# Performance work log

Hardware: AMD Instinct MI355X
Metric: run time of the kernel (lower is better)

The kernel has to match this reference:

```python
import jax, jax.numpy as jnp
import numpy as np

DIM = 2048
N_HEADS = 16
N_KV_HEADS = 4
HEAD_DIM = DIM // N_HEADS  # 128
T = 2048


def setup_inputs() -> dict:
    key = jax.random.key(0)
    k1, k2, k3 = jax.random.split(key, 3)
    scale = 1.0 / np.sqrt(DIM)
    x = jax.random.normal(k1, (T, DIM), dtype=jnp.float32)
    # GQA-consistent fused QKV projection: q (n_h*hd) + k (n_kv*hd) + v (n_kv*hd)
    qkv_out = (N_HEADS + 2 * N_KV_HEADS) * HEAD_DIM  # 3072
    W_qkv = jax.random.normal(k2, (DIM, qkv_out), dtype=jnp.float32) * scale
    W_o = jax.random.normal(k3, (N_HEADS * HEAD_DIM, DIM), dtype=jnp.float32) * scale
    return {"x": x, "W_qkv": W_qkv, "W_o": W_o}


def reference(x, W_qkv, W_o):
    Tn, C = x.shape
    hd = HEAD_DIM
    qkv = x @ W_qkv  # [T, (n_h + 2*n_kv)*hd]
    q, k, v = jnp.split(qkv, [N_HEADS * hd, (N_HEADS + N_KV_HEADS) * hd], axis=-1)
    q = q.reshape(Tn, N_HEADS, hd).transpose(1, 0, 2)      # [n_h, T, hd]
    k = k.reshape(Tn, N_KV_HEADS, hd).transpose(1, 0, 2)   # [n_kv, T, hd]
    v = v.reshape(Tn, N_KV_HEADS, hd).transpose(1, 0, 2)
    rep = N_HEADS // N_KV_HEADS
    k = jnp.repeat(k, rep, axis=0)  # [n_h, T, hd]
    v = jnp.repeat(v, rep, axis=0)
    scores = jnp.einsum('hid,hjd->hij', q, k) / jnp.sqrt(jnp.asarray(hd, x.dtype))
    causal = jnp.tril(jnp.ones((Tn, Tn), dtype=bool))[None, :, :]
    scores = jnp.where(causal, scores, -jnp.inf)
    attn = jax.nn.softmax(scores, axis=-1)
    out = jnp.einsum('hij,hjd->hid', attn, v)  # [n_h, T, hd]
    out = out.transpose(1, 0, 2).reshape(Tn, N_HEADS * hd)
    return out @ W_o
```

## Files before the change

### kernel.cpp

```cpp
#include <hip/hip_runtime.h>
#include <stdint.h>

#define T_SEQ   2048
#define DMODEL  2048
#define NH      16
#define HD      128
#define QKVN    3072
#define KCOL    2048
#define VCOL    2560

typedef __bf16 bf16x8 __attribute__((ext_vector_type(8)));
typedef float  f32x4  __attribute__((ext_vector_type(4)));
typedef unsigned short u16x8 __attribute__((ext_vector_type(8)));

__device__ __forceinline__ uint16_t f2bf(float f) {
    uint32_t u = __builtin_bit_cast(uint32_t, f);
    u += 0x7fffu + ((u >> 16) & 1u);
    return (uint16_t)(u >> 16);
}
__device__ __forceinline__ float bf2f(uint16_t u) {
    return __builtin_bit_cast(float, (uint32_t)u << 16);
}
__device__ __forceinline__ u16x8 ld8(const uint16_t* p) {
    return *reinterpret_cast<const u16x8*>(p);
}
__device__ __forceinline__ void st8(uint16_t* p, u16x8 v) {
    *reinterpret_cast<u16x8*>(p) = v;
}
__device__ __forceinline__ bf16x8 as_bf(u16x8 v) { return __builtin_bit_cast(bf16x8, v); }

__device__ __forceinline__ uint32_t cvtpk(float a, float b) {
    uint32_t r;
    asm("v_cvt_pk_bf16_f32 %0, %1, %2" : "=v"(r) : "v"(a), "v"(b));
    return r;
}

__device__ __forceinline__ void gl_lds16(const uint16_t* g, uint16_t* l) {
    __builtin_amdgcn_global_load_lds((const __attribute__((address_space(1))) void*)g,
                                     (__attribute__((address_space(3))) void*)l, 16, 0, 0);
}

__global__ __launch_bounds__(256) void k_cast(const float* __restrict__ in,
                                              uint16_t* __restrict__ out, int n8) {
    int i = blockIdx.x * 256 + threadIdx.x;
    if (i >= n8) return;
    const f32x4* p = reinterpret_cast<const f32x4*>(in) + (size_t)i * 2;
    f32x4 a = p[0], b = p[1];
    u16x8 o;
    o[0] = f2bf(a[0]); o[1] = f2bf(a[1]); o[2] = f2bf(a[2]); o[3] = f2bf(a[3]);
    o[4] = f2bf(b[0]); o[5] = f2bf(b[1]); o[6] = f2bf(b[2]); o[7] = f2bf(b[3]);
    reinterpret_cast<u16x8*>(out)[i] = o;
}

__global__ __launch_bounds__(256) void k_tcast(const float* __restrict__ in,
                                               uint16_t* __restrict__ out, int R, int C) {
    __shared__ uint16_t tile[64][72];
    int t = threadIdx.x;
    int rbase = blockIdx.y * 64, cbase = blockIdx.x * 64;
#pragma unroll
    for (int p = 0; p < 4; ++p) {
        int ir = p * 16 + (t >> 4);
        int ic = (t & 15) * 4;
        f32x4 v = *reinterpret_cast<const f32x4*>(&in[(size_t)(rbase + ir) * C + cbase + ic]);
        tile[ir][ic + 0] = f2bf(v[0]);
        tile[ir][ic + 1] = f2bf(v[1]);
        tile[ir][ic + 2] = f2bf(v[2]);
        tile[ir][ic + 3] = f2bf(v[3]);
    }
    __syncthreads();
#pragma unroll
    for (int p = 0; p < 2; ++p) {
        int oc = p * 32 + (t >> 3);
        int orr = (t & 7) * 8;
        u16x8 o;
#pragma unroll
        for (int e = 0; e < 8; ++e) o[e] = tile[orr + e][oc];
        st8(&out[(size_t)(cbase + oc) * R + rbase + orr], o);
    }
}

__global__ __launch_bounds__(256) void k_tbf16(const uint16_t* __restrict__ in,
                                               uint16_t* __restrict__ out,
                                               int R, int C, int ldin, int coff) {
    __shared__ uint16_t tile[64][72];
    int t = threadIdx.x;
    int rbase = blockIdx.y * 64, cbase = blockIdx.x * 64;
#pragma unroll
    for (int p = 0; p < 2; ++p) {
        int ir = p * 32 + (t >> 3);
        int ic = (t & 7) * 8;
        u16x8 v = ld8(&in[(size_t)(rbase + ir) * ldin + coff + cbase + ic]);
#pragma unroll
        for (int e = 0; e < 8; ++e) tile[ir][ic + e] = v[e];
    }
    __syncthreads();
#pragma unroll
    for (int p = 0; p < 2; ++p) {
        int oc = p * 32 + (t >> 3);
        int orr = (t & 7) * 8;
        u16x8 o;
#pragma unroll
        for (int e = 0; e < 8; ++e) o[e] = tile[orr + e][oc];
        st8(&out[(size_t)(cbase + oc) * R + rbase + orr], o);
    }
}

__global__ __launch_bounds__(256) void k_gemm(const uint16_t* __restrict__ A,
                                              const uint16_t* __restrict__ Bt,
                                              void* __restrict__ Cout,
                                              int M, int N, int K, int gy,
                                              int out_bf16, int scale_cols, float qscale) {
    __shared__ __align__(16) uint16_t Asm[2][64 * 64];
    __shared__ __align__(16) uint16_t Bsm[2][128 * 64];
    int t = threadIdx.x;
    int w = t >> 6, lane = t & 63, lo = lane & 15, g4 = lane >> 4;

    int nwg = (int)gridDim.x;
    int wg = (int)blockIdx.x;
    int idx = (wg & 7) * (nwg >> 3) + (wg >> 3);
    int bx = idx / gy, by = idx % gy;
    int mbase = by * 64, nbase = bx * 128;

    int wm = w >> 1, wn = w & 1;

    const uint16_t* pA[2]; int lofsA[2];
#pragma unroll
    for (int c = 0; c < 2; ++c) {
        int ch = w * 2 + c;
        int r = ch * 8 + (lane >> 3);
        pA[c] = A + (size_t)(mbase + r) * K + (((lane & 7) ^ (r & 7)) * 8);
        lofsA[c] = ch * 512;
    }
    const uint16_t* pB[4]; int lofsB[4];
#pragma unroll
    for (int c = 0; c < 4; ++c) {
        int ch = w * 4 + c;
        int r = ch * 8 + (lane >> 3);
        pB[c] = Bt + (size_t)(nbase + r) * K + (((lane & 7) ^ (r & 7)) * 8);
        lofsB[c] = ch * 512;
    }

    f32x4 acc[2][4] = {};

#pragma unroll
    for (int c = 0; c < 2; ++c) gl_lds16(pA[c], &Asm[0][lofsA[c]]);
#pragma unroll
    for (int c = 0; c < 4; ++c) gl_lds16(pB[c], &Bsm[0][lofsB[c]]);

    int cur = 0;
    for (int kt = 0; kt < K; kt += 64) {
        __syncthreads();
        if (kt + 64 < K) {
            int ko = kt + 64;
#pragma unroll
            for (int c = 0; c < 2; ++c) gl_lds16(pA[c] + ko, &Asm[cur ^ 1][lofsA[c]]);
#pragma unroll
            for (int c = 0; c < 4; ++c) gl_lds16(pB[c] + ko, &Bsm[cur ^ 1][lofsB[c]]);
        }
        bf16x8 af[2][2], bfr[2][4];
#pragma unroll
        for (int ks = 0; ks < 2; ++ks) {
#pragma unroll
            for (int i = 0; i < 2; ++i) {
                int ar = wm * 32 + i * 16 + lo;
                af[ks][i] = as_bf(ld8(&Asm[cur][(ar * 64 + ks * 32 + g4 * 8) ^ ((lo & 7) << 3)]));
            }
#pragma unroll
            for (int j = 0; j < 4; ++j) {
                int br = wn * 64 + j * 16 + lo;
                bfr[ks][j] = as_bf(ld8(&Bsm[cur][(br * 64 + ks * 32 + g4 * 8) ^ ((lo & 7) << 3)]));
            }
        }
        __builtin_amdgcn_s_setprio(1);
#pragma unroll
        for (int ks = 0; ks < 2; ++ks)
#pragma unroll
            for (int i = 0; i < 2; ++i)
#pragma unroll
                for (int j = 0; j < 4; ++j)
                    acc[i][j] = __builtin_amdgcn_mfma_f32_16x16x32_bf16(af[ks][i], bfr[ks][j], acc[i][j], 0, 0, 0);
        __builtin_amdgcn_s_setprio(0);
        cur ^= 1;
    }

    if (out_bf16) {
        uint16_t* C = (uint16_t*)Cout;
#pragma unroll
        for (int i = 0; i < 2; ++i)
#pragma unroll
            for (int j = 0; j < 4; ++j)
#pragma unroll
                for (int r = 0; r < 4; ++r) {
                    int row = mbase + wm * 32 + i * 16 + g4 * 4 + r;
                    int col = nbase + wn * 64 + j * 16 + lo;
                    float v = acc[i][j][r];
                    if (col < scale_cols) v *= qscale;
                    C[(size_t)row * N + col] = f2bf(v);
                }
    } else {
        float* C = (float*)Cout;
#pragma unroll
        for (int i = 0; i < 2; ++i)
#pragma unroll
            for (int j = 0; j < 4; ++j)
#pragma unroll
                for (int r = 0; r < 4; ++r) {
                    int row = mbase + wm * 32 + i * 16 + g4 * 4 + r;
                    int col = nbase + wn * 64 + j * 16 + lo;
                    C[(size_t)row * N + col] = acc[i][j][r];
                }
    }
}

__global__ __launch_bounds__(256) void k_attn(const uint16_t* __restrict__ qkv,
                                              const uint16_t* __restrict__ vt,
                                              uint16_t* __restrict__ po,
                                              float* __restrict__ pml) {
    __shared__ __align__(16) uint16_t Ksm[2][64 * 128];
    __shared__ __align__(16) uint16_t Vsm[2][128 * 64];
    __shared__ __align__(16) uint16_t Psm[4][16 * 72];
    int t = threadIdx.x;
    int w = t >> 6, lane = t & 63, lo = lane & 15, g4 = lane >> 4;
    int x = blockIdx.x, h = blockIdx.y, p = blockIdx.z, kh = h >> 2;

    const uint16_t* kbase = qkv + KCOL + (size_t)kh * HD;
    const uint16_t* vbase = vt + (size_t)(kh * HD) * T_SEQ;

    const uint16_t* kp[4]; const uint16_t* vp[4]; int lofs[4];
#pragma unroll
    for (int c = 0; c < 4; ++c) {
        int ch = w * 4 + c;
        int kr = ch * 4 + (lane >> 4);
        kp[c] = kbase + (size_t)kr * QKVN + ((lane & 15) ^ (kr & 7)) * 8;
        int vr = ch * 8 + (lane >> 3);
        vp[c] = vbase + (size_t)vr * T_SEQ + ((lane & 7) ^ (vr & 7)) * 8;
        lofs[c] = ch * 512;
    }

    for (int rep = 0; rep < 2; ++rep) {
        int qt = rep ? 31 - x : x;
        int qb = qt * 64;
        int cnt = (qt + 2 - p) >> 1;

        bf16x8 qf[4];
        {
            int qrow = qb + w * 16 + lo;
            const uint16_t* qp = &qkv[(size_t)qrow * QKVN + h * HD + g4 * 8];
#pragma unroll
            for (int ks = 0; ks < 4; ++ks) qf[ks] = as_bf(ld8(qp + ks * 32));
        }

        f32x4 o[8] = {};
        float mr = -INFINITY, pp = 0.f;

        if (cnt) {
            __syncthreads();
            size_t ko = (size_t)p * 64 * QKVN; int vo = p * 64;
#pragma unroll
            for (int c = 0; c < 4; ++c) {
                gl_lds16(kp[c] + ko, &Ksm[0][lofs[c]]);
                gl_lds16(vp[c] + vo, &Vsm[0][lofs[c]]);
            }
        }

        int cur = 0;
        for (int it = 0; it < cnt; ++it) {
            int jt = p + 2 * it;
            __syncthreads();
            if (it + 1 < cnt) {
                size_t ko = (size_t)(jt + 2) * 64 * QKVN;
                int vo = (jt + 2) * 64;
#pragma unroll
                for (int c = 0; c < 4; ++c) {
                    gl_lds16(kp[c] + ko, &Ksm[cur ^ 1][lofs[c]]);
                    gl_lds16(vp[c] + vo, &Vsm[cur ^ 1][lofs[c]]);
                }
            }

            f32x4 s[4] = {};
            __builtin_amdgcn_s_setprio(1);
#pragma unroll
            for (int nt = 0; nt < 4; ++nt) {
                int j = nt * 16 + lo;
#pragma unroll
                for (int ks = 0; ks < 4; ++ks) {
                    bf16x8 a = as_bf(ld8(&Ksm[cur][(j * 128 + ks * 32 + g4 * 8) ^ ((lo & 7) << 3)]));
                    s[nt] = __builtin_amdgcn_mfma_f32_16x16x32_bf16(a, qf[ks], s[nt], 0, 0, 0);
                }
            }
            __builtin_amdgcn_s_setprio(0);

            if (jt == qt) {
                int i = qb + w * 16 + lo;
                int jb = jt * 64;
#pragma unroll
                for (int nt = 0; nt < 4; ++nt)
#pragma unroll
                    for (int r = 0; r < 4; ++r) {
                        int j = jb + nt * 16 + g4 * 4 + r;
                        if (j > i) s[nt][r] = -INFINITY;
                    }
            }

            float pm = fmaxf(
                fmaxf(fmaxf(fmaxf(s[0][0], s[0][1]), fmaxf(s[0][2], s[0][3])),
                      fmaxf(fmaxf(s[1][0], s[1][1]), fmaxf(s[1][2], s[1][3]))),
                fmaxf(fmaxf(fmaxf(s[2][0], s[2][1]), fmaxf(s[2][2], s[2][3])),
                      fmaxf(fmaxf(s[3][0], s[3][1]), fmaxf(s[3][2], s[3][3]))));
            pm = fmaxf(pm, __shfl_xor(pm, 16));
            pm = fmaxf(pm, __shfl_xor(pm, 32));

            if (__any(pm > mr + 11.f)) {
                float mn = fmaxf(mr, pm);
                float al = exp2f(fminf(fmaxf(mr, -1e30f) - mn, 0.f));
                mr = mn;
                pp *= al;
                float alo[4];
#pragma unroll
                for (int r = 0; r < 4; ++r)
                    alo[r] = __shfl(al, (lane & 48) | (((lane >> 4) << 2) + r));
#pragma unroll
                for (int dt = 0; dt < 8; ++dt)
#pragma unroll
                    for (int r = 0; r < 4; ++r) o[dt][r] *= alo[r];
            }
            float msafe = fmaxf(mr, -1e30f);
#pragma unroll
            for (int nt = 0; nt < 4; ++nt)
#pragma unroll
                for (int r = 0; r < 4; ++r) {
                    float pe = exp2f(s[nt][r] - msafe);
                    s[nt][r] = pe;
                    pp += pe;
                }
#pragma unroll
            for (int nt = 0; nt < 4; ++nt) {
                uint32_t p01 = cvtpk(s[nt][0], s[nt][1]);
                uint32_t p23 = cvtpk(s[nt][2], s[nt][3]);
                *reinterpret_cast<uint2*>(&Psm[w][lo * 72 + nt * 16 + g4 * 4]) =
                    make_uint2(p01, p23);
            }

            __builtin_amdgcn_s_setprio(1);
#pragma unroll
            for (int ks2 = 0; ks2 < 2; ++ks2) {
                bf16x8 pa = as_bf(ld8(&Psm[w][lo * 72 + ks2 * 32 + g4 * 8]));
#pragma unroll
                for (int dt = 0; dt < 8; ++dt) {
                    int d = dt * 16 + lo;
                    bf16x8 vb = as_bf(ld8(&Vsm[cur][(d * 64 + ks2 * 32 + g4 * 8) ^ ((lo & 7) << 3)]));
                    o[dt] = __builtin_amdgcn_mfma_f32_16x16x32_bf16(pa, vb, o[dt], 0, 0, 0);
                }
            }
            __builtin_amdgcn_s_setprio(0);
            cur ^= 1;
        }

        float lr = pp;
        lr += __shfl_xor(lr, 16);
        lr += __shfl_xor(lr, 32);

        uint16_t* pob = po + (size_t)p * T_SEQ * DMODEL;
#pragma unroll
        for (int dt = 0; dt < 8; ++dt)
#pragma unroll
            for (int r = 0; r < 4; ++r) {
                int i = qb + w * 16 + g4 * 4 + r;
                int col = h * HD + dt * 16 + lo;
                pob[(size_t)i * DMODEL + col] = f2bf(o[dt][r]);
            }
        if (lane < 16) {
            int i = qb + w * 16 + lane;
            float* pe = pml + (size_t)p * T_SEQ * NH * 2 + ((size_t)i * NH + h) * 2;
            pe[0] = mr;
            pe[1] = lr;
        }
    }
}

__global__ __launch_bounds__(256) void k_comb(uint16_t* __restrict__ po,
                                              const float* __restrict__ pml) {
    int i = blockIdx.x * 256 + threadIdx.x;
    int row = i >> 8;
    int cg = i & 255;
    int h = cg >> 4;
    int col = cg * 8;
    const size_t PS = (size_t)T_SEQ * NH * 2;
    const size_t TD = (size_t)T_SEQ * DMODEL;
    size_t mo = ((size_t)row * NH + h) * 2;
    float m0 = pml[mo], l0 = pml[mo + 1];
    float m1 = pml[PS + mo], l1 = pml[PS + mo + 1];
    float m = fmaxf(m0, m1);
    float w0 = exp2f(m0 - m), w1 = exp2f(m1 - m);
    float rl = 1.f / (l0 * w0 + l1 * w1);
    size_t off = (size_t)row * DMODEL + col;
    u16x8 a = ld8(po + off);
    u16x8 b = ld8(po + TD + off);
    u16x8 o;
#pragma unroll
    for (int e = 0; e < 8; ++e)
        o[e] = f2bf((bf2f(a[e]) * w0 + bf2f(b[e]) * w1) * rl);
    st8(po + off, o);
}

extern "C" void kernel_launch(void* const* d_in, const int* in_sizes, int n_in,
                              void* d_out, int out_size, void* d_ws, size_t ws_size,
                              hipStream_t stream) {
    (void)in_sizes; (void)n_in; (void)out_size; (void)ws_size;
    const float* x    = (const float*)d_in[0];
    const float* Wqkv = (const float*)d_in[1];
    const float* Wo   = (const float*)d_in[2];
    float* out = (float*)d_out;

    char* ws = (char*)d_ws;
    uint16_t* xb   = (uint16_t*)(ws + 0);
    uint16_t* wqt  = (uint16_t*)(ws + 8388608);
    uint16_t* po   = (uint16_t*)(ws + 0);
    float*    pml  = (float*)(ws + 16777216);
    uint16_t* wot  = (uint16_t*)(ws + 20971520);
    uint16_t* qkvb = (uint16_t*)(ws + 29360128);
    uint16_t* vtb  = (uint16_t*)(ws + 41943040);

    const float qscale = 0.12751743f;

    k_cast<<<2048, 256, 0, stream>>>(x, xb, 524288);
    k_tcast<<<dim3(48, 32), 256, 0, stream>>>(Wqkv, wqt, 2048, 3072);
    k_tcast<<<dim3(32, 32), 256, 0, stream>>>(Wo, wot, 2048, 2048);
    k_gemm<<<768, 256, 0, stream>>>(xb, wqt, qkvb, 2048, 3072, 2048, 32, 1, 2048, qscale);
    k_tbf16<<<dim3(8, 32), 256, 0, stream>>>(qkvb, vtb, 2048, 512, 3072, 2560);
    k_attn<<<dim3(16, 16, 2), 256, 0, stream>>>(qkvb, vtb, po, pml);
    k_comb<<<2048, 256, 0, stream>>>(po, pml);
    k_gemm<<<512, 256, 0, stream>>>(po, wot, out, 2048, 2048, 2048, 32, 0, 0, 1.0f);
}
```

Before: 133.7 us.

## Triple-buffer GEMM LDS with K-tile 32 and vmcnt-based barrier

Changes the GEMM's shared-memory pipeline from double buffering with 64-wide K tiles to triple buffering with 32-wide K tiles. Loads now run two stages ahead, and the full __syncthreads is replaced by a partial s_waitcnt vmcnt(3) plus a raw barrier. The swizzle is redone for the narrower 32-element rows. The goal is to hide global-load latency better while using less LDS per block. The cost is twice as many loop iterations and barriers per K, with fewer MFMAs between each sync.

```diff
diff --git a/kernel.cpp b/kernel.cpp
--- a/kernel.cpp
+++ b/kernel.cpp
@@ -110,8 +110,8 @@
                                               void* __restrict__ Cout,
                                               int M, int N, int K, int gy,
                                               int out_bf16, int scale_cols, float qscale) {
-    __shared__ __align__(16) uint16_t Asm[2][64 * 64];
-    __shared__ __align__(16) uint16_t Bsm[2][128 * 64];
+    __shared__ __align__(16) uint16_t Asm[3][64 * 32];
+    __shared__ __align__(16) uint16_t Bsm[3][128 * 32];
     int t = threadIdx.x;
     int w = t >> 6, lane = t & 63, lo = lane & 15, g4 = lane >> 4;
 
@@ -123,64 +123,79 @@
 
     int wm = w >> 1, wn = w & 1;
 
-    const uint16_t* pA[2]; int lofsA[2];
+    int rA = w * 16 + (lane >> 2);
+    const uint16_t* pA = A + (size_t)(mbase + rA) * K + (((lane & 3) ^ ((rA >> 1) & 3)) * 8);
+    int lofsA = w * 512;
+    const uint16_t* pB[2]; int lofsB[2];
 #pragma unroll
     for (int c = 0; c < 2; ++c) {
         int ch = w * 2 + c;
-        int r = ch * 8 + (lane >> 3);
-        pA[c] = A + (size_t)(mbase + r) * K + (((lane & 7) ^ (r & 7)) * 8);
-        lofsA[c] = ch * 512;
-    }
-    const uint16_t* pB[4]; int lofsB[4];
-#pragma unroll
-    for (int c = 0; c < 4; ++c) {
-        int ch = w * 4 + c;
-        int r = ch * 8 + (lane >> 3);
-        pB[c] = Bt + (size_t)(nbase + r) * K + (((lane & 7) ^ (r & 7)) * 8);
+        int r = ch * 16 + (lane >> 2);
+        pB[c] = Bt + (size_t)(nbase + r) * K + (((lane & 3) ^ ((r >> 1) & 3)) * 8);
         lofsB[c] = ch * 512;
     }
 
     f32x4 acc[2][4] = {};
-
-#pragma unroll
-    for (int c = 0; c < 2; ++c) gl_lds16(pA[c], &Asm[0][lofsA[c]]);
-#pragma unroll
-    for (int c = 0; c < 4; ++c) gl_lds16(pB[c], &Bsm[0][lofsB[c]]);
-
-    int cur = 0;
-    for (int kt = 0; kt < K; kt += 64) {
-        __syncthreads();
-        if (kt + 64 < K) {
-            int ko = kt + 64;
-#pragma unroll
-            for (int c = 0; c < 2; ++c) gl_lds16(pA[c] + ko, &Asm[cur ^ 1][lofsA[c]]);
-#pragma unroll
-            for (int c = 0; c < 4; ++c) gl_lds16(pB[c] + ko, &Bsm[cur ^ 1][lofsB[c]]);
-        }
-        bf16x8 af[2][2], bfr[2][4];
-#pragma unroll
-        for (int ks = 0; ks < 2; ++ks) {
-#pragma unroll
-            for (int i = 0; i < 2; ++i) {
-                int ar = wm * 32 + i * 16 + lo;
-                af[ks][i] = as_bf(ld8(&Asm[cur][(ar * 64 + ks * 32 + g4 * 8) ^ ((lo & 7) << 3)]));
-            }
-#pragma unroll
-            for (int j = 0; j < 4; ++j) {
-                int br = wn * 64 + j * 16 + lo;
-                bfr[ks][j] = as_bf(ld8(&Bsm[cur][(br * 64 + ks * 32 + g4 * 8) ^ ((lo & 7) << 3)]));
-            }
+    int nt = K >> 5;
+
+    gl_lds16(pA, &Asm[0][lofsA]);
+    gl_lds16(pB[0], &Bsm[0][lofsB[0]]); gl_lds16(pB[1], &Bsm[0][lofsB[1]]);
+    gl_lds16(pA + 32, &Asm[1][lofsA]);
+    gl_lds16(pB[0] + 32, &Bsm[1][lofsB[0]]); gl_lds16(pB[1] + 32, &Bsm[1][lofsB[1]]);
+
+    int cur = 0, st = 2;
+    for (int tt = 0; tt < nt - 1; ++tt) {
+        asm volatile("s_waitcnt vmcnt(3)" ::: "memory");
+        __builtin_amdgcn_s_barrier();
+        asm volatile("" ::: "memory");
+        if (tt + 2 < nt) {
+            int ko = (tt + 2) * 32;
+            gl_lds16(pA + ko, &Asm[st][lofsA]);
+            gl_lds16(pB[0] + ko, &Bsm[st][lofsB[0]]);
+            gl_lds16(pB[1] + ko, &Bsm[st][lofsB[1]]);
+        }
+        bf16x8 af[2], bfr[4];
+#pragma unroll
+        for (int i = 0; i < 2; ++i) {
+            int ar = wm * 32 + i * 16 + lo;
+            af[i] = as_bf(ld8(&Asm[cur][(ar * 32 + g4 * 8) ^ (((ar >> 1) & 3) << 3)]));
+        }
+#pragma unroll
+        for (int j = 0; j < 4; ++j) {
+            int br = wn * 64 + j * 16 + lo;
+            bfr[j] = as_bf(ld8(&Bsm[cur][(br * 32 + g4 * 8) ^ (((br >> 1) & 3) << 3)]));
         }
         __builtin_amdgcn_s_setprio(1);
 #pragma unroll
-        for (int ks = 0; ks < 2; ++ks)
-#pragma unroll
-            for (int i = 0; i < 2; ++i)
-#pragma unroll
-                for (int j = 0; j < 4; ++j)
-                    acc[i][j] = __builtin_amdgcn_mfma_f32_16x16x32_bf16(af[ks][i], bfr[ks][j], acc[i][j], 0, 0, 0);
+        for (int i = 0; i < 2; ++i)
+#pragma unroll
+            for (int j = 0; j < 4; ++j)
+                acc[i][j] = __builtin_amdgcn_mfma_f32_16x16x32_bf16(af[i], bfr[j], acc[i][j], 0, 0, 0);
         __builtin_amdgcn_s_setprio(0);
-        cur ^= 1;
+        asm volatile("" ::: "memory");
+        cur = (cur == 2) ? 0 : cur + 1;
+        st  = (st  == 2) ? 0 : st  + 1;
+    }
+    asm volatile("s_waitcnt vmcnt(0)" ::: "memory");
+    __builtin_amdgcn_s_barrier();
+    asm volatile("" ::: "memory");
+    {
+        bf16x8 af[2], bfr[4];
+#pragma unroll
+        for (int i = 0; i < 2; ++i) {
+            int ar = wm * 32 + i * 16 + lo;
+            af[i] = as_bf(ld8(&Asm[cur][(ar * 32 + g4 * 8) ^ (((ar >> 1) & 3) << 3)]));
+        }
+#pragma unroll
+        for (int j = 0; j < 4; ++j) {
+            int br = wn * 64 + j * 16 + lo;
+            bfr[j] = as_bf(ld8(&Bsm[cur][(br * 32 + g4 * 8) ^ (((br >> 1) & 3) << 3)]));
+        }
+#pragma unroll
+        for (int i = 0; i < 2; ++i)
+#pragma unroll
+            for (int j = 0; j < 4; ++j)
+                acc[i][j] = __builtin_amdgcn_mfma_f32_16x16x32_bf16(af[i], bfr[j], acc[i][j], 0, 0, 0);
     }
 
     if (out_bf16) {
```

Result: slower. 146.1 us (+9.3%).

## Enlarge attention query tile to 128 rows per block with single-buffered K

Applied to the files above, without the earlier changes.

Each attention block now covers 128 query rows, with each wave owning two 16-row halves, instead of looping over two balanced 64-row tiles. Every K/V tile loaded into shared memory now serves twice as many queries, which cuts shared-memory and global traffic per unit of work. K drops to a single buffer that is refilled after an extra mid-iteration barrier, and the PV MFMA operands are swapped so output stores are vectorized. In exchange, register pressure roughly doubles for the accumulators, blocks no longer get balanced causal work (heaviest blocks are scheduled first), and the added barrier may expose K load latency.

```diff
diff --git a/kernel.cpp b/kernel.cpp
--- a/kernel.cpp
+++ b/kernel.cpp
@@ -216,12 +216,15 @@
                                               const uint16_t* __restrict__ vt,
                                               uint16_t* __restrict__ po,
                                               float* __restrict__ pml) {
-    __shared__ __align__(16) uint16_t Ksm[2][64 * 128];
+    __shared__ __align__(16) uint16_t Ksm[64 * 128];
     __shared__ __align__(16) uint16_t Vsm[2][128 * 64];
-    __shared__ __align__(16) uint16_t Psm[4][16 * 72];
+    __shared__ __align__(16) uint16_t Psm[4][32 * 72];
     int t = threadIdx.x;
     int w = t >> 6, lane = t & 63, lo = lane & 15, g4 = lane >> 4;
-    int x = blockIdx.x, h = blockIdx.y, p = blockIdx.z, kh = h >> 2;
+    int qt1 = 15 - (int)blockIdx.x;
+    int h = blockIdx.y, p = blockIdx.z, kh = h >> 2;
+    int qb = qt1 * 128;
+    int qwb = w * 32;
 
     const uint16_t* kbase = qkv + KCOL + (size_t)kh * HD;
     const uint16_t* vbase = vt + (size_t)(kh * HD) * T_SEQ;
@@ -237,143 +240,165 @@
         lofs[c] = ch * 512;
     }
 
-    for (int rep = 0; rep < 2; ++rep) {
-        int qt = rep ? 31 - x : x;
-        int qb = qt * 64;
-        int cnt = (qt + 2 - p) >> 1;
-
-        bf16x8 qf[4];
-        {
-            int qrow = qb + w * 16 + lo;
-            const uint16_t* qp = &qkv[(size_t)qrow * QKVN + h * HD + g4 * 8];
-#pragma unroll
-            for (int ks = 0; ks < 4; ++ks) qf[ks] = as_bf(ld8(qp + ks * 32));
-        }
-
-        f32x4 o[8] = {};
-        float mr = -INFINITY, pp = 0.f;
-
-        if (cnt) {
-            __syncthreads();
-            size_t ko = (size_t)p * 64 * QKVN; int vo = p * 64;
-#pragma unroll
-            for (int c = 0; c < 4; ++c) {
-                gl_lds16(kp[c] + ko, &Ksm[0][lofs[c]]);
-                gl_lds16(vp[c] + vo, &Vsm[0][lofs[c]]);
-            }
-        }
-
-        int cur = 0;
-        for (int it = 0; it < cnt; ++it) {
-            int jt = p + 2 * it;
-            __syncthreads();
-            if (it + 1 < cnt) {
-                size_t ko = (size_t)(jt + 2) * 64 * QKVN;
-                int vo = (jt + 2) * 64;
-#pragma unroll
-                for (int c = 0; c < 4; ++c) {
-                    gl_lds16(kp[c] + ko, &Ksm[cur ^ 1][lofs[c]]);
-                    gl_lds16(vp[c] + vo, &Vsm[cur ^ 1][lofs[c]]);
-                }
-            }
-
-            f32x4 s[4] = {};
-            __builtin_amdgcn_s_setprio(1);
-#pragma unroll
-            for (int nt = 0; nt < 4; ++nt) {
-                int j = nt * 16 + lo;
-#pragma unroll
-                for (int ks = 0; ks < 4; ++ks) {
-                    bf16x8 a = as_bf(ld8(&Ksm[cur][(j * 128 + ks * 32 + g4 * 8) ^ ((lo & 7) << 3)]));
-                    s[nt] = __builtin_amdgcn_mfma_f32_16x16x32_bf16(a, qf[ks], s[nt], 0, 0, 0);
-                }
-            }
-            __builtin_amdgcn_s_setprio(0);
-
-            if (jt == qt) {
-                int i = qb + w * 16 + lo;
-                int jb = jt * 64;
-#pragma unroll
-                for (int nt = 0; nt < 4; ++nt)
+    bf16x8 qf[2][4];
+#pragma unroll
+    for (int qh = 0; qh < 2; ++qh) {
+        const uint16_t* qp = &qkv[(size_t)(qb + qwb + qh * 16 + lo) * QKVN + h * HD + g4 * 8];
+#pragma unroll
+        for (int ks = 0; ks < 4; ++ks) qf[qh][ks] = as_bf(ld8(qp + ks * 32));
+    }
+
+    f32x4 o[2][8] = {};
+    float mr[2] = {-INFINITY, -INFINITY}, pp[2] = {0.f, 0.f};
+    int cnt = qt1 + 1;
+
+    {
+        size_t ko = (size_t)p * 64 * QKVN; int vo = p * 64;
+#pragma unroll
+        for (int c = 0; c < 4; ++c) {
+            gl_lds16(kp[c] + ko, &Ksm[lofs[c]]);
+            gl_lds16(vp[c] + vo, &Vsm[0][lofs[c]]);
+        }
+    }
+
+    int cur = 0;
+    for (int it = 0; it < cnt; ++it) {
+        int jt = p + 2 * it;
+        __syncthreads();
+        if (it + 1 < cnt) {
+            int vo = (jt + 2) * 64;
+#pragma unroll
+            for (int c = 0; c < 4; ++c) gl_lds16(vp[c] + vo, &Vsm[cur ^ 1][lofs[c]]);
+        }
+
+        f32x4 s[4][2] = {};
+        __builtin_amdgcn_s_setprio(1);
+#pragma unroll
+        for (int nt = 0; nt < 4; ++nt) {
+            int j = nt * 16 + lo;
+#pragma unroll
+            for (int ks = 0; ks < 4; ++ks) {
+                bf16x8 a = as_bf(ld8(&Ksm[(j * 128 + ks * 32 + g4 * 8) ^ ((lo & 7) << 3)]));
+                s[nt][0] = __builtin_amdgcn_mfma_f32_16x16x32_bf16(a, qf[0][ks], s[nt][0], 0, 0, 0);
+                s[nt][1] = __builtin_amdgcn_mfma_f32_16x16x32_bf16(a, qf[1][ks], s[nt][1], 0, 0, 0);
+            }
+        }
+        __builtin_amdgcn_s_setprio(0);
+
+        asm volatile("" ::: "memory");
+        __builtin_amdgcn_s_barrier();
+        asm volatile("" ::: "memory");
+        if (it + 1 < cnt) {
+            size_t ko = (size_t)(jt + 2) * 64 * QKVN;
+#pragma unroll
+            for (int c = 0; c < 4; ++c) gl_lds16(kp[c] + ko, &Ksm[lofs[c]]);
+        }
+
+        if (jt >= 2 * qt1) {
+            int jb = jt * 64;
+#pragma unroll
+            for (int nt = 0; nt < 4; ++nt)
+#pragma unroll
+                for (int qh = 0; qh < 2; ++qh) {
+                    int i = qb + qwb + qh * 16 + lo;
 #pragma unroll
                     for (int r = 0; r < 4; ++r) {
                         int j = jb + nt * 16 + g4 * 4 + r;
-                        if (j > i) s[nt][r] = -INFINITY;
+                        if (j > i) s[nt][qh][r] = -INFINITY;
                     }
-            }
-
-            float pm = fmaxf(
-                fmaxf(fmaxf(fmaxf(s[0][0], s[0][1]), fmaxf(s[0][2], s[0][3])),
-                      fmaxf(fmaxf(s[1][0], s[1][1]), fmaxf(s[1][2], s[1][3]))),
-                fmaxf(fmaxf(fmaxf(s[2][0], s[2][1]), fmaxf(s[2][2], s[2][3])),
-                      fmaxf(fmaxf(s[3][0], s[3][1]), fmaxf(s[3][2], s[3][3]))));
-            pm = fmaxf(pm, __shfl_xor(pm, 16));
-            pm = fmaxf(pm, __shfl_xor(pm, 32));
-
-            if (__any(pm > mr + 11.f)) {
-                float mn = fmaxf(mr, pm);
-                float al = exp2f(fminf(fmaxf(mr, -1e30f) - mn, 0.f));
-                mr = mn;
-                pp *= al;
-                float alo[4];
-#pragma unroll
-                for (int r = 0; r < 4; ++r)
-                    alo[r] = __shfl(al, (lane & 48) | (((lane >> 4) << 2) + r));
-#pragma unroll
-                for (int dt = 0; dt < 8; ++dt)
-#pragma unroll
-                    for (int r = 0; r < 4; ++r) o[dt][r] *= alo[r];
-            }
-            float msafe = fmaxf(mr, -1e30f);
+                }
+        }
+
+        float pm[2];
+#pragma unroll
+        for (int qh = 0; qh < 2; ++qh) {
+            float m01 = fmaxf(fmaxf(fmaxf(s[0][qh][0], s[0][qh][1]), fmaxf(s[0][qh][2], s[0][qh][3])),
+                              fmaxf(fmaxf(s[1][qh][0], s[1][qh][1]), fmaxf(s[1][qh][2], s[1][qh][3])));
+            float m23 = fmaxf(fmaxf(fmaxf(s[2][qh][0], s[2][qh][1]), fmaxf(s[2][qh][2], s[2][qh][3])),
+                              fmaxf(fmaxf(s[3][qh][0], s[3][qh][1]), fmaxf(s[3][qh][2], s[3][qh][3])));
+            float pmv = fmaxf(m01, m23);
+            pmv = fmaxf(pmv, __shfl_xor(pmv, 16));
+            pmv = fmaxf(pmv, __shfl_xor(pmv, 32));
+            pm[qh] = pmv;
+        }
+        bool grow = (pm[0] > mr[0] + 11.f) || (pm[1] > mr[1] + 11.f);
+        if (__any(grow)) {
+#pragma unroll
+            for (int qh = 0; qh < 2; ++qh) {
+                float mn = fmaxf(mr[qh], pm[qh]);
+                float al = exp2f(fminf(fmaxf(mr[qh], -1e30f) - mn, 0.f));
+                mr[qh] = mn;
+                pp[qh] *= al;
+#pragma unroll
+                for (int dt = 0; dt < 8; ++dt) o[qh][dt] *= al;
+            }
+        }
+#pragma unroll
+        for (int qh = 0; qh < 2; ++qh) {
+            float msafe = fmaxf(mr[qh], -1e30f);
 #pragma unroll
             for (int nt = 0; nt < 4; ++nt)
 #pragma unroll
                 for (int r = 0; r < 4; ++r) {
-                    float pe = exp2f(s[nt][r] - msafe);
-                    s[nt][r] = pe;
-                    pp += pe;
+                    float pe = exp2f(s[nt][qh][r] - msafe);
+                    s[nt][qh][r] = pe;
+                    pp[qh] += pe;
                 }
+        }
+#pragma unroll
+        for (int qh = 0; qh < 2; ++qh)
 #pragma unroll
             for (int nt = 0; nt < 4; ++nt) {
-                uint32_t p01 = cvtpk(s[nt][0], s[nt][1]);
-                uint32_t p23 = cvtpk(s[nt][2], s[nt][3]);
-                *reinterpret_cast<uint2*>(&Psm[w][lo * 72 + nt * 16 + g4 * 4]) =
+                uint32_t p01 = cvtpk(s[nt][qh][0], s[nt][qh][1]);
+                uint32_t p23 = cvtpk(s[nt][qh][2], s[nt][qh][3]);
+                *reinterpret_cast<uint2*>(&Psm[w][(qh * 16 + lo) * 72 + nt * 16 + g4 * 4]) =
                     make_uint2(p01, p23);
             }
 
-            __builtin_amdgcn_s_setprio(1);
-#pragma unroll
-            for (int ks2 = 0; ks2 < 2; ++ks2) {
-                bf16x8 pa = as_bf(ld8(&Psm[w][lo * 72 + ks2 * 32 + g4 * 8]));
-#pragma unroll
-                for (int dt = 0; dt < 8; ++dt) {
-                    int d = dt * 16 + lo;
-                    bf16x8 vb = as_bf(ld8(&Vsm[cur][(d * 64 + ks2 * 32 + g4 * 8) ^ ((lo & 7) << 3)]));
-                    o[dt] = __builtin_amdgcn_mfma_f32_16x16x32_bf16(pa, vb, o[dt], 0, 0, 0);
-                }
-            }
-            __builtin_amdgcn_s_setprio(0);
-            cur ^= 1;
-        }
-
-        float lr = pp;
-        lr += __shfl_xor(lr, 16);
-        lr += __shfl_xor(lr, 32);
-
-        uint16_t* pob = po + (size_t)p * T_SEQ * DMODEL;
-#pragma unroll
-        for (int dt = 0; dt < 8; ++dt)
-#pragma unroll
-            for (int r = 0; r < 4; ++r) {
-                int i = qb + w * 16 + g4 * 4 + r;
-                int col = h * HD + dt * 16 + lo;
-                pob[(size_t)i * DMODEL + col] = f2bf(o[dt][r]);
-            }
-        if (lane < 16) {
-            int i = qb + w * 16 + lane;
+        __builtin_amdgcn_s_setprio(1);
+#pragma unroll
+        for (int ks2 = 0; ks2 < 2; ++ks2) {
+            bf16x8 pa0 = as_bf(ld8(&Psm[w][(lo) * 72 + ks2 * 32 + g4 * 8]));
+            bf16x8 pa1 = as_bf(ld8(&Psm[w][(16 + lo) * 72 + ks2 * 32 + g4 * 8]));
+#pragma unroll
+            for (int dt = 0; dt < 8; ++dt) {
+                int d = dt * 16 + lo;
+                bf16x8 vb = as_bf(ld8(&Vsm[cur][(d * 64 + ks2 * 32 + g4 * 8) ^ ((lo & 7) << 3)]));
+                o[0][dt] = __builtin_amdgcn_mfma_f32_16x16x32_bf16(vb, pa0, o[0][dt], 0, 0, 0);
+                o[1][dt] = __builtin_amdgcn_mfma_f32_16x16x32_bf16(vb, pa1, o[1][dt], 0, 0, 0);
+            }
+        }
+        __builtin_amdgcn_s_setprio(0);
+        cur ^= 1;
+    }
+
+    float lr[2];
+#pragma unroll
+    for (int qh = 0; qh < 2; ++qh) {
+        float ps = pp[qh];
+        ps += __shfl_xor(ps, 16);
+        ps += __shfl_xor(ps, 32);
+        lr[qh] = ps;
+    }
+
+    uint16_t* pob = po + (size_t)p * T_SEQ * DMODEL;
+#pragma unroll
+    for (int qh = 0; qh < 2; ++qh) {
+        size_t rowo = (size_t)(qb + qwb + qh * 16 + lo) * DMODEL + h * HD + g4 * 4;
+#pragma unroll
+        for (int dt = 0; dt < 8; ++dt) {
+            uint32_t c01 = cvtpk(o[qh][dt][0], o[qh][dt][1]);
+            uint32_t c23 = cvtpk(o[qh][dt][2], o[qh][dt][3]);
+            *reinterpret_cast<uint2*>(&pob[rowo + dt * 16]) = make_uint2(c01, c23);
+        }
+    }
+    if (lane < 16) {
+#pragma unroll
+        for (int qh = 0; qh < 2; ++qh) {
+            int i = qb + qwb + qh * 16 + lane;
             float* pe = pml + (size_t)p * T_SEQ * NH * 2 + ((size_t)i * NH + h) * 2;
-            pe[0] = mr;
-            pe[1] = lr;
+            pe[0] = mr[qh];
+            pe[1] = lr[qh];
         }
     }
 }
```

Measured after the change: 171.7 us. 28.5% more time.

## Rework attention to 128-row Q tiles with 32x32 MFMA and 4-way KV split

Applied to the files above, without the earlier changes.

The attention kernel now processes 128 query rows per block, 32 per wave, using 32x32x16 bf16 MFMA instead of 16x16x32. The key dimension is split four ways instead of two, and the split order is reversed on the second pass to balance causal work. K now uses a single LDS buffer reloaded after a mid-iteration barrier, while V stays double-buffered. The combine kernel merges four partials, and the workspace layout is reshuffled, with the Wo transpose moved later so its buffer can overlap freed space. Larger tiles improve reuse of K/V loads, at the cost of more partial-output traffic, an extra barrier per iteration and more registers per thread.

```diff
diff --git a/kernel.cpp b/kernel.cpp
--- a/kernel.cpp
+++ b/kernel.cpp
@@ -11,6 +11,7 @@
 
 typedef __bf16 bf16x8 __attribute__((ext_vector_type(8)));
 typedef float  f32x4  __attribute__((ext_vector_type(4)));
+typedef float  f32x16 __attribute__((ext_vector_type(16)));
 typedef unsigned short u16x8 __attribute__((ext_vector_type(8)));
 
 __device__ __forceinline__ uint16_t f2bf(float f) {
@@ -216,11 +217,12 @@
                                               const uint16_t* __restrict__ vt,
                                               uint16_t* __restrict__ po,
                                               float* __restrict__ pml) {
-    __shared__ __align__(16) uint16_t Ksm[2][64 * 128];
+    __shared__ __align__(16) uint16_t Ksm[64 * 128];
     __shared__ __align__(16) uint16_t Vsm[2][128 * 64];
-    __shared__ __align__(16) uint16_t Psm[4][16 * 72];
+    __shared__ __align__(16) uint16_t Psm[4][32 * 72];
     int t = threadIdx.x;
-    int w = t >> 6, lane = t & 63, lo = lane & 15, g4 = lane >> 4;
+    int w = t >> 6, lane = t & 63;
+    int q32 = lane & 31, hi = lane >> 5;
     int x = blockIdx.x, h = blockIdx.y, p = blockIdx.z, kh = h >> 2;
 
     const uint16_t* kbase = qkv + KCOL + (size_t)kh * HD;
@@ -238,76 +240,80 @@
     }
 
     for (int rep = 0; rep < 2; ++rep) {
-        int qt = rep ? 31 - x : x;
-        int qb = qt * 64;
-        int cnt = (qt + 2 - p) >> 1;
-
-        bf16x8 qf[4];
+        int qt = rep ? 15 - x : x;
+        int pr = rep ? 3 - p : p;
+        int qb = qt * 128;
+        int cnt = (2 * qt + 5 - pr) >> 2;
+
+        bf16x8 qf[8];
         {
-            int qrow = qb + w * 16 + lo;
-            const uint16_t* qp = &qkv[(size_t)qrow * QKVN + h * HD + g4 * 8];
-#pragma unroll
-            for (int ks = 0; ks < 4; ++ks) qf[ks] = as_bf(ld8(qp + ks * 32));
-        }
-
-        f32x4 o[8] = {};
+            const uint16_t* qp = &qkv[(size_t)(qb + w * 32 + q32) * QKVN + h * HD + hi * 8];
+#pragma unroll
+            for (int ks = 0; ks < 8; ++ks) qf[ks] = as_bf(ld8(qp + ks * 16));
+        }
+
+        f32x16 o[4] = {};
         float mr = -INFINITY, pp = 0.f;
 
         if (cnt) {
             __syncthreads();
-            size_t ko = (size_t)p * 64 * QKVN; int vo = p * 64;
+            size_t ko = (size_t)pr * 64 * QKVN; int vo = pr * 64;
 #pragma unroll
             for (int c = 0; c < 4; ++c) {
-                gl_lds16(kp[c] + ko, &Ksm[0][lofs[c]]);
+                gl_lds16(kp[c] + ko, &Ksm[lofs[c]]);
                 gl_lds16(vp[c] + vo, &Vsm[0][lofs[c]]);
             }
         }
 
         int cur = 0;
         for (int it = 0; it < cnt; ++it) {
-            int jt = p + 2 * it;
+            int jt = pr + 4 * it;
             __syncthreads();
             if (it + 1 < cnt) {
-                size_t ko = (size_t)(jt + 2) * 64 * QKVN;
-                int vo = (jt + 2) * 64;
-#pragma unroll
-                for (int c = 0; c < 4; ++c) {
-                    gl_lds16(kp[c] + ko, &Ksm[cur ^ 1][lofs[c]]);
-                    gl_lds16(vp[c] + vo, &Vsm[cur ^ 1][lofs[c]]);
+                int vo = (jt + 4) * 64;
+#pragma unroll
+                for (int c = 0; c < 4; ++c) gl_lds16(vp[c] + vo, &Vsm[cur ^ 1][lofs[c]]);
+            }
+
+            f32x16 s0 = {}, s1 = {};
+            __builtin_amdgcn_s_setprio(1);
+#pragma unroll
+            for (int ks = 0; ks < 8; ++ks) {
+                int j0 = q32;
+                bf16x8 k0 = as_bf(ld8(&Ksm[(j0 * 128 + ks * 16 + hi * 8) ^ ((j0 & 7) << 3)]));
+                s0 = __builtin_amdgcn_mfma_f32_32x32x16_bf16(k0, qf[ks], s0, 0, 0, 0);
+                int j1 = 32 + q32;
+                bf16x8 k1 = as_bf(ld8(&Ksm[(j1 * 128 + ks * 16 + hi * 8) ^ ((j1 & 7) << 3)]));
+                s1 = __builtin_amdgcn_mfma_f32_32x32x16_bf16(k1, qf[ks], s1, 0, 0, 0);
+            }
+            __builtin_amdgcn_s_setprio(0);
+
+            asm volatile("" ::: "memory");
+            __builtin_amdgcn_s_barrier();
+            asm volatile("" ::: "memory");
+            if (it + 1 < cnt) {
+                size_t ko = (size_t)(jt + 4) * 64 * QKVN;
+#pragma unroll
+                for (int c = 0; c < 4; ++c) gl_lds16(kp[c] + ko, &Ksm[lofs[c]]);
+            }
+
+            if (jt >= 2 * qt) {
+                int i = qb + w * 32 + q32;
+                int jb = jt * 64;
+#pragma unroll
+                for (int r = 0; r < 16; ++r) {
+                    int jr = jb + (r & 3) + 8 * (r >> 2) + 4 * hi;
+                    if (jr > i) s0[r] = -INFINITY;
+                    if (jr + 32 > i) s1[r] = -INFINITY;
                 }
             }
 
-            f32x4 s[4] = {};
-            __builtin_amdgcn_s_setprio(1);
-#pragma unroll
-            for (int nt = 0; nt < 4; ++nt) {
-                int j = nt * 16 + lo;
-#pragma unroll
-                for (int ks = 0; ks < 4; ++ks) {
-                    bf16x8 a = as_bf(ld8(&Ksm[cur][(j * 128 + ks * 32 + g4 * 8) ^ ((lo & 7) << 3)]));
-                    s[nt] = __builtin_amdgcn_mfma_f32_16x16x32_bf16(a, qf[ks], s[nt], 0, 0, 0);
-                }
-            }
-            __builtin_amdgcn_s_setprio(0);
-
-            if (jt == qt) {
-                int i = qb + w * 16 + lo;
-                int jb = jt * 64;
-#pragma unroll
-                for (int nt = 0; nt < 4; ++nt)
-#pragma unroll
-                    for (int r = 0; r < 4; ++r) {
-                        int j = jb + nt * 16 + g4 * 4 + r;
-                        if (j > i) s[nt][r] = -INFINITY;
-                    }
-            }
-
-            float pm = fmaxf(
-                fmaxf(fmaxf(fmaxf(s[0][0], s[0][1]), fmaxf(s[0][2], s[0][3])),
-                      fmaxf(fmaxf(s[1][0], s[1][1]), fmaxf(s[1][2], s[1][3]))),
-                fmaxf(fmaxf(fmaxf(s[2][0], s[2][1]), fmaxf(s[2][2], s[2][3])),
-                      fmaxf(fmaxf(s[3][0], s[3][1]), fmaxf(s[3][2], s[3][3]))));
-            pm = fmaxf(pm, __shfl_xor(pm, 16));
+            float t8[8];
+#pragma unroll
+            for (int r = 0; r < 8; ++r)
+                t8[r] = fmaxf(fmaxf(s0[r], s0[r + 8]), fmaxf(s1[r], s1[r + 8]));
+            float pm = fmaxf(fmaxf(fmaxf(t8[0], t8[1]), fmaxf(t8[2], t8[3])),
+                             fmaxf(fmaxf(t8[4], t8[5]), fmaxf(t8[6], t8[7])));
             pm = fmaxf(pm, __shfl_xor(pm, 32));
 
             if (__any(pm > mr + 11.f)) {
@@ -315,63 +321,68 @@
                 float al = exp2f(fminf(fmaxf(mr, -1e30f) - mn, 0.f));
                 mr = mn;
                 pp *= al;
-                float alo[4];
-#pragma unroll
-                for (int r = 0; r < 4; ++r)
-                    alo[r] = __shfl(al, (lane & 48) | (((lane >> 4) << 2) + r));
-#pragma unroll
-                for (int dt = 0; dt < 8; ++dt)
-#pragma unroll
-                    for (int r = 0; r < 4; ++r) o[dt][r] *= alo[r];
+                float alo[16];
+#pragma unroll
+                for (int r = 0; r < 16; ++r)
+                    alo[r] = __shfl(al, (r & 3) + 8 * (r >> 2) + 4 * hi);
+#pragma unroll
+                for (int nt = 0; nt < 4; ++nt)
+#pragma unroll
+                    for (int r = 0; r < 16; ++r) o[nt][r] *= alo[r];
             }
             float msafe = fmaxf(mr, -1e30f);
-#pragma unroll
-            for (int nt = 0; nt < 4; ++nt)
-#pragma unroll
-                for (int r = 0; r < 4; ++r) {
-                    float pe = exp2f(s[nt][r] - msafe);
-                    s[nt][r] = pe;
-                    pp += pe;
-                }
-#pragma unroll
-            for (int nt = 0; nt < 4; ++nt) {
-                uint32_t p01 = cvtpk(s[nt][0], s[nt][1]);
-                uint32_t p23 = cvtpk(s[nt][2], s[nt][3]);
-                *reinterpret_cast<uint2*>(&Psm[w][lo * 72 + nt * 16 + g4 * 4]) =
-                    make_uint2(p01, p23);
+            float ppa = 0.f, ppb = 0.f;
+#pragma unroll
+            for (int r = 0; r < 16; ++r) {
+                float e0 = exp2f(s0[r] - msafe);
+                s0[r] = e0; ppa += e0;
+                float e1 = exp2f(s1[r] - msafe);
+                s1[r] = e1; ppb += e1;
+            }
+            pp += ppa + ppb;
+
+#pragma unroll
+            for (int g = 0; g < 4; ++g) {
+                uint32_t a01 = cvtpk(s0[4 * g], s0[4 * g + 1]);
+                uint32_t a23 = cvtpk(s0[4 * g + 2], s0[4 * g + 3]);
+                *reinterpret_cast<uint2*>(&Psm[w][q32 * 72 + 8 * g + 4 * hi]) =
+                    make_uint2(a01, a23);
+                uint32_t b01 = cvtpk(s1[4 * g], s1[4 * g + 1]);
+                uint32_t b23 = cvtpk(s1[4 * g + 2], s1[4 * g + 3]);
+                *reinterpret_cast<uint2*>(&Psm[w][q32 * 72 + 32 + 8 * g + 4 * hi]) =
+                    make_uint2(b01, b23);
             }
 
             __builtin_amdgcn_s_setprio(1);
 #pragma unroll
-            for (int ks2 = 0; ks2 < 2; ++ks2) {
-                bf16x8 pa = as_bf(ld8(&Psm[w][lo * 72 + ks2 * 32 + g4 * 8]));
-#pragma unroll
-                for (int dt = 0; dt < 8; ++dt) {
-                    int d = dt * 16 + lo;
-                    bf16x8 vb = as_bf(ld8(&Vsm[cur][(d * 64 + ks2 * 32 + g4 * 8) ^ ((lo & 7) << 3)]));
-                    o[dt] = __builtin_amdgcn_mfma_f32_16x16x32_bf16(pa, vb, o[dt], 0, 0, 0);
+            for (int ks2 = 0; ks2 < 4; ++ks2) {
+                bf16x8 pa = as_bf(ld8(&Psm[w][q32 * 72 + ks2 * 16 + hi * 8]));
+#pragma unroll
+                for (int nt = 0; nt < 4; ++nt) {
+                    int d = nt * 32 + q32;
+                    bf16x8 vb = as_bf(ld8(&Vsm[cur][(d * 64 + ks2 * 16 + hi * 8) ^ ((d & 7) << 3)]));
+                    o[nt] = __builtin_amdgcn_mfma_f32_32x32x16_bf16(pa, vb, o[nt], 0, 0, 0);
                 }
             }
             __builtin_amdgcn_s_setprio(0);
             cur ^= 1;
         }
 
-        float lr = pp;
-        lr += __shfl_xor(lr, 16);
-        lr += __shfl_xor(lr, 32);
-
-        uint16_t* pob = po + (size_t)p * T_SEQ * DMODEL;
-#pragma unroll
-        for (int dt = 0; dt < 8; ++dt)
-#pragma unroll
-            for (int r = 0; r < 4; ++r) {
-                int i = qb + w * 16 + g4 * 4 + r;
-                int col = h * HD + dt * 16 + lo;
-                pob[(size_t)i * DMODEL + col] = f2bf(o[dt][r]);
-            }
-        if (lane < 16) {
-            int i = qb + w * 16 + lane;
-            float* pe = pml + (size_t)p * T_SEQ * NH * 2 + ((size_t)i * NH + h) * 2;
+        float lr = pp + __shfl_xor(pp, 32);
+
+        uint16_t* pob = po + (size_t)pr * T_SEQ * DMODEL;
+#pragma unroll
+        for (int nt = 0; nt < 4; ++nt)
+#pragma unroll
+            for (int r = 0; r < 16; ++r) {
+                int ql = (r & 3) + 8 * (r >> 2) + 4 * hi;
+                int i = qb + w * 32 + ql;
+                int col = h * HD + nt * 32 + q32;
+                pob[(size_t)i * DMODEL + col] = f2bf(o[nt][r]);
+            }
+        if (hi == 0) {
+            int i = qb + w * 32 + q32;
+            float* pe = pml + (size_t)pr * T_SEQ * NH * 2 + ((size_t)i * NH + h) * 2;
             pe[0] = mr;
             pe[1] = lr;
         }
@@ -388,18 +399,22 @@
     const size_t PS = (size_t)T_SEQ * NH * 2;
     const size_t TD = (size_t)T_SEQ * DMODEL;
     size_t mo = ((size_t)row * NH + h) * 2;
-    float m0 = pml[mo], l0 = pml[mo + 1];
-    float m1 = pml[PS + mo], l1 = pml[PS + mo + 1];
-    float m = fmaxf(m0, m1);
-    float w0 = exp2f(m0 - m), w1 = exp2f(m1 - m);
-    float rl = 1.f / (l0 * w0 + l1 * w1);
+    float m0 = pml[mo],          l0 = pml[mo + 1];
+    float m1 = pml[PS + mo],     l1 = pml[PS + mo + 1];
+    float m2 = pml[2 * PS + mo], l2 = pml[2 * PS + mo + 1];
+    float m3 = pml[3 * PS + mo], l3 = pml[3 * PS + mo + 1];
+    float m = fmaxf(fmaxf(m0, m1), fmaxf(m2, m3));
+    float w0 = exp2f(m0 - m), w1 = exp2f(m1 - m), w2 = exp2f(m2 - m), w3 = exp2f(m3 - m);
+    float rl = 1.f / (l0 * w0 + l1 * w1 + l2 * w2 + l3 * w3);
     size_t off = (size_t)row * DMODEL + col;
     u16x8 a = ld8(po + off);
     u16x8 b = ld8(po + TD + off);
+    u16x8 c = ld8(po + 2 * TD + off);
+    u16x8 d = ld8(po + 3 * TD + off);
     u16x8 o;
 #pragma unroll
     for (int e = 0; e < 8; ++e)
-        o[e] = f2bf((bf2f(a[e]) * w0 + bf2f(b[e]) * w1) * rl);
+        o[e] = f2bf((bf2f(a[e]) * w0 + bf2f(b[e]) * w1 + bf2f(c[e]) * w2 + bf2f(d[e]) * w3) * rl);
     st8(po + off, o);
 }
 
@@ -416,19 +431,19 @@
     uint16_t* xb   = (uint16_t*)(ws + 0);
     uint16_t* wqt  = (uint16_t*)(ws + 8388608);
     uint16_t* po   = (uint16_t*)(ws + 0);
-    float*    pml  = (float*)(ws + 16777216);
-    uint16_t* wot  = (uint16_t*)(ws + 20971520);
-    uint16_t* qkvb = (uint16_t*)(ws + 29360128);
-    uint16_t* vtb  = (uint16_t*)(ws + 41943040);
+    float*    pml  = (float*)(ws + 33554432);
+    uint16_t* qkvb = (uint16_t*)(ws + 34603008);
+    uint16_t* vtb  = (uint16_t*)(ws + 47185920);
+    uint16_t* wot  = (uint16_t*)(ws + 8388608);
 
     const float qscale = 0.12751743f;
 
     k_cast<<<2048, 256, 0, stream>>>(x, xb, 524288);
     k_tcast<<<dim3(48, 32), 256, 0, stream>>>(Wqkv, wqt, 2048, 3072);
-    k_tcast<<<dim3(32, 32), 256, 0, stream>>>(Wo, wot, 2048, 2048);
     k_gemm<<<768, 256, 0, stream>>>(xb, wqt, qkvb, 2048, 3072, 2048, 32, 1, 2048, qscale);
     k_tbf16<<<dim3(8, 32), 256, 0, stream>>>(qkvb, vtb, 2048, 512, 3072, 2560);
-    k_attn<<<dim3(16, 16, 2), 256, 0, stream>>>(qkvb, vtb, po, pml);
+    k_attn<<<dim3(8, 16, 4), 256, 0, stream>>>(qkvb, vtb, po, pml);
     k_comb<<<2048, 256, 0, stream>>>(po, pml);
+    k_tcast<<<dim3(32, 32), 256, 0, stream>>>(Wo, wot, 2048, 2048);
     k_gemm<<<512, 256, 0, stream>>>(po, wot, out, 2048, 2048, 2048, 32, 0, 0, 1.0f);
 }
```

New measurement: 144.1 us. +7.8%, slower.
